# Performance work log

Hardware: AMD Instinct MI355X
Metric: run time of the kernel (lower is better)

The kernel has to match this reference:

```python
import jax, jax.numpy as jnp
import numpy as np

D_MODEL = 512
N_HEADS = 8
D_KV = 64
EPS = 1e-6
ROPE_THETA = 10000.0


def _rms_norm(x, w):
    # T5-style RMSNorm: no mean subtraction, no bias, variance in fp32.
    var = jnp.mean(x.astype(jnp.float32) ** 2, axis=-1, keepdims=True)
    return (x * jax.lax.rsqrt(var + EPS)).astype(x.dtype) * w


def _rope_cos_sin(pos, dk):
    # pos: [B, T] int -> cos/sin: [B, 1, T, dk]
    inv_freq = 1.0 / (ROPE_THETA ** (jnp.arange(0, dk, 2, dtype=jnp.float32) / dk))
    ang = pos.astype(jnp.float32)[:, :, None] * inv_freq[None, None, :]  # [B,T,dk/2]
    ang = jnp.concatenate([ang, ang], axis=-1)                            # [B,T,dk]
    return jnp.cos(ang)[:, None], jnp.sin(ang)[:, None]


def _rotate_half(x):
    h = x.shape[-1] // 2
    return jnp.concatenate([-x[..., h:], x[..., :h]], axis=-1)


def _mha(x, mask, wq, wk, wv, wo, pos=None):
    # x: [B, T, D]; mask: [B, H, T, T] additive
    B, T, _ = x.shape
    def proj(w):
        return (x @ w).reshape(B, T, N_HEADS, D_KV).transpose(0, 2, 1, 3)  # [B,H,T,dk]
    q, k, v = proj(wq), proj(wk), proj(wv)
    if pos is not None:
        cos, sin = _rope_cos_sin(pos, D_KV)
        cos, sin = cos.astype(x.dtype), sin.astype(x.dtype)
        q = q * cos + _rotate_half(q) * sin
        k = k * cos + _rotate_half(k) * sin
    scale = 1.0 / np.sqrt(D_KV)
    scores = jnp.einsum('bhqd,bhkd->bhqk', q, k) * scale + mask
    attn = jax.nn.softmax(scores.astype(jnp.float32), axis=-1).astype(scores.dtype)
    out = jnp.einsum('bhqk,bhkd->bhqd', attn, v)
    out = out.transpose(0, 2, 1, 3).reshape(B, T, N_HEADS * D_KV)
    return out @ wo


def setup_inputs() -> dict:
    key = jax.random.key(0)
    ks = jax.random.split(key, 12)
    B, T = 8, 1024
    s = 1.0 / np.sqrt(D_MODEL)
    inp = {
        'h': jax.random.normal(ks[0], (B, T, D_MODEL), dtype=jnp.float32),
        'pos': jnp.broadcast_to(jnp.arange(T, dtype=jnp.int64 if jax.config.jax_enable_x64 else jnp.int32)[None, :], (B, T)),
        't_mask': jnp.zeros((B, N_HEADS, T, T), dtype=jnp.float32),
        'g_mask': jnp.zeros((T, N_HEADS, B, B), dtype=jnp.float32),
        'ln_t_w': jnp.ones((D_MODEL,), dtype=jnp.float32),
        'ln_g_w': jnp.ones((D_MODEL,), dtype=jnp.float32),
    }
    names = ['wq_t', 'wk_t', 'wv_t', 'wo_t', 'wq_g', 'wk_g', 'wv_g', 'wo_g']
    for i, n in enumerate(names):
        inp[n] = jax.random.normal(ks[i + 1], (D_MODEL, D_MODEL), dtype=jnp.float32) * s
    return inp


def reference(h, pos, t_mask, g_mask, ln_t_w, ln_g_w,
              wq_t, wk_t, wv_t, wo_t, wq_g, wk_g, wv_g, wo_g):
    # --- time attention (over T axis, with RoPE) ---
    normed = _rms_norm(h, ln_t_w)
    attn_t = _mha(normed, t_mask, wq_t, wk_t, wv_t, wo_t, pos=pos)
    h = h + attn_t  # dropout p=0 (eval)
    # --- group attention (over B axis, no RoPE) ---
    h = h.transpose(1, 0, 2)  # [T, B, D]
    normed = _rms_norm(h, ln_g_w)
    attn_g = _mha(normed, g_mask, wq_g, wk_g, wv_g, wo_g, pos=None)
    h = h + attn_g
    return h.transpose(1, 0, 2)  # back to [B, T, D]
```

## Files before the change

kernel.cpp:

```cpp
#include <hip/hip_runtime.h>
#include <hip/hip_bf16.h>
#include <math.h>


typedef __bf16 bf16x8 __attribute__((ext_vector_type(8)));
typedef __bf16 bf16x4 __attribute__((ext_vector_type(4)));
typedef float  f32x4  __attribute__((ext_vector_type(4)));

#define LN1E4_OVER_32 0.2878231366242558f

__device__ __forceinline__ void gld16(const void* g, void* l) {
    __builtin_amdgcn_global_load_lds((const __attribute__((address_space(1))) void*)g,
                                     (__attribute__((address_space(3))) void*)l,
                                     16, 0, 0);
}

__device__ __forceinline__ int swz64(int r, int c) {
    return r * 64 + (((c + r) & 7) << 3);
}

__global__ __launch_bounds__(256) void prep_k(
    const float* __restrict__ x, const float* __restrict__ wln, __bf16* __restrict__ y,
    const float* w0, const float* w1, const float* w2, const float* w3,
    const float* w4, const float* w5, const float* w6, const float* w7,
    const float* __restrict__ gln, float* __restrict__ rmsbuf,
    __bf16* qkvT_t, __bf16* oT_t, __bf16* qkvT_g, __bf16* oT_g)
{
    __shared__ float tile[32][33];
    int bid = blockIdx.x;
    if (bid < 2048) {
        if (bid < 32) rmsbuf[bid * 256 + threadIdx.x] = 0.0f;
        int row = bid * 4 + (threadIdx.x >> 6);
        int l = threadIdx.x & 63;
        const float* xr = x + (size_t)row * 512 + l * 8;
        float4 a = *(const float4*)xr;
        float4 b = *(const float4*)(xr + 4);
        float ss = a.x*a.x + a.y*a.y + a.z*a.z + a.w*a.w
                 + b.x*b.x + b.y*b.y + b.z*b.z + b.w*b.w;
        for (int m = 1; m < 64; m <<= 1) ss += __shfl_xor(ss, m);
        float rms = rsqrtf(ss * (1.0f / 512.0f) + 1e-6f);
        float4 wa = *(const float4*)(wln + l * 8);
        float4 wb = *(const float4*)(wln + l * 8 + 4);
        bf16x8 o;
        o[0] = (__bf16)(a.x * rms * wa.x); o[1] = (__bf16)(a.y * rms * wa.y);
        o[2] = (__bf16)(a.z * rms * wa.z); o[3] = (__bf16)(a.w * rms * wa.w);
        o[4] = (__bf16)(b.x * rms * wb.x); o[5] = (__bf16)(b.y * rms * wb.y);
        o[6] = (__bf16)(b.z * rms * wb.z); o[7] = (__bf16)(b.w * rms * wb.w);
        *(bf16x8*)(y + (size_t)row * 512 + l * 8) = o;
        return;
    }
    int bid2 = bid - 2048;
    int mat = bid2 >> 8, rem = bid2 & 255;
    const float* src; __bf16* dst; int rowOff;
    switch (mat) {
        case 0: src=w0; dst=qkvT_t; rowOff=0;    break;
        case 1: src=w1; dst=qkvT_t; rowOff=512;  break;
        case 2: src=w2; dst=qkvT_t; rowOff=1024; break;
        case 3: src=w3; dst=oT_t;   rowOff=0;    break;
        case 4: src=w4; dst=qkvT_g; rowOff=0;    break;
        case 5: src=w5; dst=qkvT_g; rowOff=512;  break;
        case 6: src=w6; dst=qkvT_g; rowOff=1024; break;
        default: src=w7; dst=oT_g;  rowOff=0;    break;
    }
    bool foldG = (mat >= 4 && mat <= 6);
    int n0 = (rem & 15) * 32, k0 = (rem >> 4) * 32;
    int tt = threadIdx.x;
    int kr = tt >> 3, nc = (tt & 7) * 4;
    float4 v = *(const float4*)(src + (size_t)(k0 + kr) * 512 + n0 + nc);
    tile[kr][nc+0] = v.x; tile[kr][nc+1] = v.y; tile[kr][nc+2] = v.z; tile[kr][nc+3] = v.w;
    __syncthreads();
    int nr = tt >> 3, kc = (tt & 7) * 4;
    float g0 = 1.f, g1 = 1.f, g2 = 1.f, g3 = 1.f;
    if (foldG) {
        float4 gv = *(const float4*)(gln + k0 + kc);
        g0 = gv.x; g1 = gv.y; g2 = gv.z; g3 = gv.w;
    }
    bf16x4 o;
    o[0] = (__bf16)(tile[kc+0][nr] * g0); o[1] = (__bf16)(tile[kc+1][nr] * g1);
    o[2] = (__bf16)(tile[kc+2][nr] * g2); o[3] = (__bf16)(tile[kc+3][nr] * g3);
    *(bf16x4*)(dst + (size_t)(rowOff + n0 + nr) * 512 + k0 + kc) = o;
}

__global__ __launch_bounds__(256) void gemm_ep(
    const __bf16* __restrict__ A, const __bf16* __restrict__ Bt,
    const int* __restrict__ pos, const float* __restrict__ rmsv,
    __bf16* __restrict__ o0, __bf16* __restrict__ o1, __bf16* __restrict__ o2,
    int mode)
{
    __shared__ __bf16 smem[16384];
    __bf16* As = smem;
    __bf16* Bs = smem + 8192;
    int tid = threadIdx.x;
    int l = tid & 63, w = tid >> 6;
    int l16 = l & 15, quad = l >> 4;
    int wm = w >> 1, wn = w & 1;
    int mblk = blockIdx.x * 128, nblk = blockIdx.y * 128;
    f32x4 acc[4][4] = {};

    for (int k0 = 0; k0 < 512; k0 += 64) {
        __syncthreads();
        #pragma unroll
        for (int i = 0; i < 4; ++i) {
            int idx = i * 256 + tid;
            int row = idx >> 3, cp = idx & 7;
            int cl = (cp - row) & 7;
            gld16(A  + (size_t)(mblk + row) * 512 + k0 + cl * 8, (char*)As + (size_t)idx * 16);
            gld16(Bt + (size_t)(nblk + row) * 512 + k0 + cl * 8, (char*)Bs + (size_t)idx * 16);
        }
        __syncthreads();
        #pragma unroll
        for (int h = 0; h < 2; h++) {
            bf16x8 aF[4], bF[4];
            #pragma unroll
            for (int mt = 0; mt < 4; mt++) aF[mt] = *(bf16x8*)(As + swz64(wm * 64 + mt * 16 + l16, h * 4 + quad));
            #pragma unroll
            for (int nt = 0; nt < 4; nt++) bF[nt] = *(bf16x8*)(Bs + swz64(wn * 64 + nt * 16 + l16, h * 4 + quad));
            #pragma unroll
            for (int mt = 0; mt < 4; mt++)
                #pragma unroll
                for (int nt = 0; nt < 4; nt++)
                    acc[mt][nt] = __builtin_amdgcn_mfma_f32_16x16x32_bf16(aF[mt], bF[nt], acc[mt][nt], 0, 0, 0);
        }
    }
    __syncthreads();

    int colbase = nblk + wn * 64;
    __bf16* bw = smem + w * 1536;
    int rbrow = l >> 3, rbch = (l & 7) * 8;

    int mat = colbase >> 9;
    int hh  = (colbase & 511) >> 6;
    __bf16* dst = (mat == 0) ? o0 : (mat == 1) ? o1 : o2;
    bool isQ = (mat == 0), isV = (mat == 2);
    if (mode == 0 && !isV) {
        float f0 = __expf((float)l16        * -LN1E4_OVER_32);
        float f1 = __expf((float)(16 + l16) * -LN1E4_OVER_32);
        #pragma unroll
        for (int mt = 0; mt < 4; mt++) {
            int grow0 = mblk + wm * 64 + mt * 16;
            int b = grow0 >> 10, t0 = grow0 & 1023;
            int4 p4 = *(const int4*)&pos[grow0 + quad * 4];
            const int pa[4] = {p4.x, p4.y, p4.z, p4.w};
            #pragma unroll
            for (int r = 0; r < 4; r++) {
                float p = (float)pa[r];
                #pragma unroll
                for (int nt = 0; nt < 2; nt++) {
                    int i = nt * 16 + l16;
                    float ang = p * (nt ? f1 : f0);
                    float c, s; __sincosf(ang, &s, &c);
                    float x1 = acc[mt][nt][r], x2 = acc[mt][nt + 2][r];
                    float y1 = x1 * c - x2 * s;
                    float y2 = x2 * c + x1 * s;
                    if (isQ) { y1 *= 0.125f; y2 *= 0.125f; }
                    bw[(quad * 4 + r) * 72 + i]      = (__bf16)y1;
                    bw[(quad * 4 + r) * 72 + i + 32] = (__bf16)y2;
                }
            }
            #pragma unroll
            for (int i = 0; i < 2; ++i) {
                int rr = rbrow + i * 8;
                bf16x8 vv = *(bf16x8*)&bw[rr * 72 + rbch];
                *(bf16x8*)&dst[((size_t)(b * 8 + hh) * 1024 + t0 + rr) * 64 + rbch] = vv;
            }
        }
    } else if (mode == 0) {
        #pragma unroll
        for (int mt = 0; mt < 4; mt++) {
            #pragma unroll
            for (int nt = 0; nt < 4; nt++)
                #pragma unroll
                for (int r = 0; r < 4; r++)
                    bw[(nt * 16 + l16) * 24 + quad * 4 + r] = (__bf16)acc[mt][nt][r];
            int grow0 = mblk + wm * 64 + mt * 16;
            int b = grow0 >> 10, t0 = grow0 & 1023;
            #pragma unroll
            for (int i = 0; i < 2; ++i) {
                int li = i * 64 + l;
                int d = li >> 1, t8 = (li & 1) * 8;
                bf16x8 vv = *(bf16x8*)&bw[d * 24 + t8];
                *(bf16x8*)&dst[((size_t)(b * 8 + hh) * 64 + d) * 1024 + t0 + t8] = vv;
            }
        }
    } else {
        #pragma unroll
        for (int mt = 0; mt < 4; mt++) {
            int grow0 = mblk + wm * 64 + mt * 16;
            f32x4 ss4 = *(const f32x4*)&rmsv[grow0 + quad * 4];
            float rsq[4];
            #pragma unroll
            for (int r = 0; r < 4; r++)
                rsq[r] = rsqrtf(ss4[r] * (1.0f / 512.0f) + 1e-6f) * (isQ ? 0.125f : 1.0f);
            #pragma unroll
            for (int nt = 0; nt < 4; nt++)
                #pragma unroll
                for (int r = 0; r < 4; r++)
                    bw[(quad * 4 + r) * 72 + nt * 16 + l16] = (__bf16)(acc[mt][nt][r] * rsq[r]);
            #pragma unroll
            for (int i = 0; i < 2; ++i) {
                int rr = rbrow + i * 8;
                int grow = grow0 + rr;
                int t = grow >> 3, bq = grow & 7;
                bf16x8 vv = *(bf16x8*)&bw[rr * 72 + rbch];
                *(bf16x8*)&dst[(((size_t)t * 8 + hh) * 8 + bq) * 64 + rbch] = vv;
            }
        }
    }
}

__global__ __launch_bounds__(256) void gemm_o(
    const __bf16* __restrict__ A, const __bf16* __restrict__ Bt,
    const float* __restrict__ resid, float* __restrict__ outF,
    __bf16* __restrict__ h2b, float* __restrict__ rmsbuf, int remap)
{
    __shared__ __align__(16) char smemraw[24576];
    __bf16* As = (__bf16*)smemraw;
    __bf16* Bs = (__bf16*)(smemraw + 8192);
    int tid = threadIdx.x;
    int l = tid & 63, w = tid >> 6;
    int l16 = l & 15, quad = l >> 4;
    int mblk = blockIdx.x * 64, nblk = blockIdx.y * 128;
    f32x4 acc[8] = {};

    for (int k0 = 0; k0 < 512; k0 += 64) {
        __syncthreads();
        #pragma unroll
        for (int i = 0; i < 2; ++i) {
            int idx = i * 256 + tid;
            int row = idx >> 3, cp = idx & 7;
            int cl = (cp - row) & 7;
            gld16(A + (size_t)(mblk + row) * 512 + k0 + cl * 8, (char*)As + (size_t)idx * 16);
        }
        #pragma unroll
        for (int i = 0; i < 4; ++i) {
            int idx = i * 256 + tid;
            int row = idx >> 3, cp = idx & 7;
            int cl = (cp - row) & 7;
            gld16(Bt + (size_t)(nblk + row) * 512 + k0 + cl * 8, (char*)Bs + (size_t)idx * 16);
        }
        __syncthreads();
        #pragma unroll
        for (int h = 0; h < 2; h++) {
            bf16x8 aF = *(bf16x8*)(As + swz64(w * 16 + l16, h * 4 + quad));
            #pragma unroll
            for (int nt = 0; nt < 8; nt++) {
                bf16x8 bF = *(bf16x8*)(Bs + swz64(nt * 16 + l16, h * 4 + quad));
                acc[nt] = __builtin_amdgcn_mfma_f32_16x16x32_bf16(aF, bF, acc[nt], 0, 0, 0);
            }
        }
    }
    __syncthreads();

    float* fw = (float*)(smemraw + w * 4352);
    int grow0 = mblk + w * 16;
    float ssq[4] = {0.f, 0.f, 0.f, 0.f};
    #pragma unroll
    for (int nh = 0; nh < 2; nh++) {
        #pragma unroll
        for (int nt = 0; nt < 4; nt++)
            #pragma unroll
            for (int r = 0; r < 4; r++)
                fw[(quad * 4 + r) * 68 + nt * 16 + l16] = acc[nh * 4 + nt][r];
        #pragma unroll
        for (int i = 0; i < 4; ++i) {
            int rr = i * 4 + (l >> 4);
            int c4 = (l & 15) * 4;
            f32x4 a4 = *(f32x4*)&fw[rr * 68 + c4];
            int grow = grow0 + rr;
            int orow = remap ? (((grow & 7) << 10) + (grow >> 3)) : grow;
            size_t oi = (size_t)orow * 512 + nblk + nh * 64 + c4;
            f32x4 r4 = *(const f32x4*)&resid[oi];
            r4 += a4;
            *(f32x4*)&outF[oi] = r4;
            if (!remap) {
                int b = grow >> 10, t = grow & 1023;
                int orow2 = t * 8 + b;
                bf16x4 h4;
                h4[0] = (__bf16)r4[0]; h4[1] = (__bf16)r4[1];
                h4[2] = (__bf16)r4[2]; h4[3] = (__bf16)r4[3];
                *(bf16x4*)&h2b[(size_t)orow2 * 512 + nblk + nh * 64 + c4] = h4;
                ssq[i] += r4[0]*r4[0] + r4[1]*r4[1] + r4[2]*r4[2] + r4[3]*r4[3];
            }
        }
    }
    if (!remap) {
        #pragma unroll
        for (int i = 0; i < 4; ++i) {
            float s = ssq[i];
            s += __shfl_xor(s, 1);
            s += __shfl_xor(s, 2);
            s += __shfl_xor(s, 4);
            s += __shfl_xor(s, 8);
            if ((l & 15) == 0) {
                int grow = grow0 + i * 4 + (l >> 4);
                int orow2 = (grow & 1023) * 8 + (grow >> 10);
                atomicAdd(&rmsbuf[orow2], s);
            }
        }
    }
}

__global__ __launch_bounds__(512) void flash_t(
    const __bf16* __restrict__ q, const __bf16* __restrict__ k,
    const __bf16* __restrict__ vt, const float* __restrict__ tmask,
    __bf16* __restrict__ ctx)
{
    int bh = blockIdx.x;
    int w = threadIdx.x >> 6, l = threadIdx.x & 63;
    int l16 = l & 15, quad = l >> 4;
    int q0 = blockIdx.y * 128 + w * 16;

    __shared__ __bf16 Ks[64 * 72];
    __shared__ __bf16 Vs[64 * 72];
    __shared__ __bf16 Ps[8][16 * 72];

    bf16x8 aQ0, aQ1;
    {
        const __bf16* qp = q + ((size_t)bh * 1024 + q0 + l16) * 64 + quad * 8;
        aQ0 = *(const bf16x8*)qp;
        aQ1 = *(const bf16x8*)(qp + 32);
    }
    f32x4 o[4] = {};
    float l_acc[4] = {0.0f, 0.0f, 0.0f, 0.0f};

    const float* mrow = tmask + (size_t)bh * 1024 * 1024 + (size_t)(q0 + quad * 4) * 1024 + l16;
    float mc[16];
    #pragma unroll
    for (int r = 0; r < 4; r++)
        #pragma unroll
        for (int nt = 0; nt < 4; nt++)
            mc[r * 4 + nt] = __builtin_nontemporal_load(mrow + (size_t)r * 1024 + nt * 16);

    for (int jb = 0; jb < 1024; jb += 64) {
        __syncthreads();
        {
            int c = threadIdx.x;
            int row = c >> 3, col = (c & 7) << 3;
            *(bf16x8*)&Ks[row * 72 + col] = *(const bf16x8*)&k [((size_t)bh * 1024 + jb + row) * 64 + col];
            *(bf16x8*)&Vs[row * 72 + col] = *(const bf16x8*)&vt[((size_t)bh * 64 + row) * 1024 + jb + col];
        }
        __syncthreads();

        float mn_[16];
        {
            int jb2 = (jb + 64) & 1023;
            const float* mr2 = mrow + jb2;
            #pragma unroll
            for (int r = 0; r < 4; r++)
                #pragma unroll
                for (int nt = 0; nt < 4; nt++)
                    mn_[r * 4 + nt] = __builtin_nontemporal_load(mr2 + (size_t)r * 1024 + nt * 16);
        }

        f32x4 s[4] = {};
        #pragma unroll
        for (int nt = 0; nt < 4; nt++) {
            bf16x8 b0 = *(bf16x8*)&Ks[(nt * 16 + l16) * 72 + quad * 8];
            bf16x8 b1 = *(bf16x8*)&Ks[(nt * 16 + l16) * 72 + 32 + quad * 8];
            s[nt] = __builtin_amdgcn_mfma_f32_16x16x32_bf16(aQ0, b0, s[nt], 0, 0, 0);
            s[nt] = __builtin_amdgcn_mfma_f32_16x16x32_bf16(aQ1, b1, s[nt], 0, 0, 0);
        }
        #pragma unroll
        for (int r = 0; r < 4; r++)
            #pragma unroll
            for (int nt = 0; nt < 4; nt++) {
                float p = __expf(s[nt][r] + mc[r * 4 + nt]);
                s[nt][r] = p;
                l_acc[r] += p;
            }

        __bf16* ps = Ps[w];
        #pragma unroll
        for (int nt = 0; nt < 4; nt++)
            #pragma unroll
            for (int r = 0; r < 4; r++)
                ps[(quad * 4 + r) * 72 + nt * 16 + l16] = (__bf16)s[nt][r];
        bf16x8 aP0 = *(bf16x8*)&ps[l16 * 72 + quad * 8];
        bf16x8 aP1 = *(bf16x8*)&ps[l16 * 72 + 32 + quad * 8];
        #pragma unroll
        for (int dt = 0; dt < 4; dt++) {
            bf16x8 bv0 = *(bf16x8*)&Vs[(dt * 16 + l16) * 72 + quad * 8];
            bf16x8 bv1 = *(bf16x8*)&Vs[(dt * 16 + l16) * 72 + 32 + quad * 8];
            o[dt] = __builtin_amdgcn_mfma_f32_16x16x32_bf16(aP0, bv0, o[dt], 0, 0, 0);
            o[dt] = __builtin_amdgcn_mfma_f32_16x16x32_bf16(aP1, bv1, o[dt], 0, 0, 0);
        }

        #pragma unroll
        for (int i = 0; i < 16; i++) mc[i] = mn_[i];
    }

    float l_i[4];
    #pragma unroll
    for (int r = 0; r < 4; r++) {
        float rs = l_acc[r];
        rs += __shfl_xor(rs, 1);
        rs += __shfl_xor(rs, 2);
        rs += __shfl_xor(rs, 4);
        rs += __shfl_xor(rs, 8);
        l_i[r] = rs;
    }

    int b = bh >> 3, h = bh & 7;
    __bf16* ps = Ps[w];
    #pragma unroll
    for (int dt = 0; dt < 4; dt++)
        #pragma unroll
        for (int r = 0; r < 4; r++)
            ps[(quad * 4 + r) * 72 + dt * 16 + l16] = (__bf16)(o[dt][r] / l_i[r]);
    int rbrow = l >> 3, rbch = (l & 7) * 8;
    #pragma unroll
    for (int i = 0; i < 2; ++i) {
        int rr = rbrow + i * 8;
        bf16x8 vv = *(bf16x8*)&ps[rr * 72 + rbch];
        *(bf16x8*)&ctx[((size_t)b * 1024 + q0 + rr) * 512 + h * 64 + rbch] = vv;
    }
}

__global__ __launch_bounds__(256) void group_attn(
    const __bf16* __restrict__ qg, const __bf16* __restrict__ kg,
    const __bf16* __restrict__ vg, const float* __restrict__ gmask,
    __bf16* __restrict__ ctxg)
{
    int tid = blockIdx.x * 256 + threadIdx.x;
    int t = tid >> 6, h = (tid >> 3) & 7, bq = tid & 7;
    size_t base = ((size_t)t * 8 + h) * 512;

    float qv[64];
    #pragma unroll
    for (int d0 = 0; d0 < 64; d0 += 8) {
        bf16x8 qq = *(const bf16x8*)&qg[base + (size_t)bq * 64 + d0];
        #pragma unroll
        for (int u = 0; u < 8; u++) qv[d0 + u] = (float)qq[u];
    }
    float s[8];
    #pragma unroll
    for (int j = 0; j < 8; j++) {
        float acc = 0.0f;
        #pragma unroll
        for (int d0 = 0; d0 < 64; d0 += 8) {
            bf16x8 kk = *(const bf16x8*)&kg[base + (size_t)j * 64 + d0];
            #pragma unroll
            for (int u = 0; u < 8; u++) acc += qv[d0 + u] * (float)kk[u];
        }
        s[j] = acc + gmask[(((size_t)t * 8 + h) * 8 + bq) * 8 + j];
    }
    float mx = s[0];
    #pragma unroll
    for (int j = 1; j < 8; j++) mx = fmaxf(mx, s[j]);
    float sum = 0.0f;
    #pragma unroll
    for (int j = 0; j < 8; j++) { s[j] = __expf(s[j] - mx); sum += s[j]; }
    float inv = 1.0f / sum;

    #pragma unroll
    for (int d0 = 0; d0 < 64; d0 += 8) {
        float o8[8] = {};
        #pragma unroll
        for (int j = 0; j < 8; j++) {
            bf16x8 vv = *(const bf16x8*)&vg[base + (size_t)j * 64 + d0];
            float pj = s[j];
            #pragma unroll
            for (int u = 0; u < 8; u++) o8[u] += pj * (float)vv[u];
        }
        bf16x8 ob;
        #pragma unroll
        for (int u = 0; u < 8; u++) ob[u] = (__bf16)(o8[u] * inv);
        *(bf16x8*)&ctxg[((size_t)t * 8 + bq) * 512 + h * 64 + d0] = ob;
    }
}

extern "C" void kernel_launch(void* const* d_in, const int* in_sizes, int n_in,
                              void* d_out, int out_size, void* d_ws, size_t ws_size,
                              hipStream_t stream)
{
    const float* h      = (const float*)d_in[0];
    const int*   pos    = (const int*)  d_in[1];
    const float* t_mask = (const float*)d_in[2];
    const float* g_mask = (const float*)d_in[3];
    const float* ln_t_w = (const float*)d_in[4];
    const float* ln_g_w = (const float*)d_in[5];
    const float* wq_t = (const float*)d_in[6];
    const float* wk_t = (const float*)d_in[7];
    const float* wv_t = (const float*)d_in[8];
    const float* wo_t = (const float*)d_in[9];
    const float* wq_g = (const float*)d_in[10];
    const float* wk_g = (const float*)d_in[11];
    const float* wv_g = (const float*)d_in[12];
    const float* wo_g = (const float*)d_in[13];
    float* out = (float*)d_out;

    char* ws = (char*)d_ws;
    const size_t MB = 1ull << 20;
    __bf16* qkvT_t = (__bf16*)ws;
    __bf16* oT_t   = qkvT_t + 786432;
    __bf16* qkvT_g = qkvT_t + 1048576;
    __bf16* oT_g   = qkvT_t + 1835008;
    __bf16* normed = (__bf16*)(ws + 4 * MB);
    __bf16* qb     = (__bf16*)(ws + 12 * MB);
    __bf16* kb     = (__bf16*)(ws + 20 * MB);
    __bf16* vb     = (__bf16*)(ws + 28 * MB);
    __bf16* ctx    = (__bf16*)(ws + 36 * MB);
    float*  h2     = (float*) (ws + 44 * MB);
    float*  rmsbuf = (float*) (ws + 60 * MB);
    __bf16* h2b    = (__bf16*)(ws + 61 * MB);

    prep_k<<<4096, 256, 0, stream>>>(h, ln_t_w, normed,
        wq_t, wk_t, wv_t, wo_t, wq_g, wk_g, wv_g, wo_g,
        ln_g_w, rmsbuf, qkvT_t, oT_t, qkvT_g, oT_g);
    gemm_ep<<<dim3(64, 12), 256, 0, stream>>>(normed, qkvT_t, pos, nullptr, qb, kb, vb, 0);
    flash_t<<<dim3(64, 8), 512, 0, stream>>>(qb, kb, vb, t_mask, ctx);
    gemm_o<<<dim3(128, 4), 256, 0, stream>>>(ctx, oT_t, h, h2, h2b, rmsbuf, 0);

    gemm_ep<<<dim3(64, 12), 256, 0, stream>>>(h2b, qkvT_g, nullptr, rmsbuf, qb, kb, vb, 2);
    group_attn<<<256, 256, 0, stream>>>(qb, kb, vb, g_mask, ctx);
    gemm_o<<<dim3(128, 4), 256, 0, stream>>>(ctx, oT_g, h2, out, nullptr, nullptr, 1);
}
```

Before: 499.0 us.

## Precompute RoPE table, prefetch K/V in flash loop, vectorize V-transpose stores

Adds extra blocks to the prep kernel that compute a cos/sin table per position, and the QKV GEMM epilogue reads it instead of evaluating sincos per element. The flash attention loop now register-prefetches the next K/V tile while the current one is processed, so global load latency overlaps compute. The V-transpose epilogue writes packed bf16x4 to shared memory, and the final normalization uses a reciprocal multiply instead of a divide. The trade-offs are extra table memory traffic in the GEMM epilogue and higher register pressure in the flash kernel.

Result: no change. 496.7 us (-0.5%).

```diff
diff --git a/kernel.cpp b/kernel.cpp
--- a/kernel.cpp
+++ b/kernel.cpp
@@ -24,7 +24,8 @@
     const float* w0, const float* w1, const float* w2, const float* w3,
     const float* w4, const float* w5, const float* w6, const float* w7,
     const float* __restrict__ gln, float* __restrict__ rmsbuf,
-    __bf16* qkvT_t, __bf16* oT_t, __bf16* qkvT_g, __bf16* oT_g)
+    __bf16* qkvT_t, __bf16* oT_t, __bf16* qkvT_g, __bf16* oT_g,
+    const int* __restrict__ pos, float2* __restrict__ rope)
 {
     __shared__ float tile[32][33];
     int bid = blockIdx.x;
@@ -49,6 +50,17 @@
         *(bf16x8*)(y + (size_t)row * 512 + l * 8) = o;
         return;
     }
+    if (bid >= 4096) {
+        int idx = bid - 4096;
+        int r = threadIdx.x >> 5, i = threadIdx.x & 31;
+        int row = idx * 8 + r;
+        float p = (float)pos[row];
+        float f = __expf((float)i * -LN1E4_OVER_32);
+        float s, c;
+        __sincosf(p * f, &s, &c);
+        rope[(size_t)row * 32 + i] = make_float2(c, s);
+        return;
+    }
     int bid2 = bid - 2048;
     int mat = bid2 >> 8, rem = bid2 & 255;
     const float* src; __bf16* dst; int rowOff;
@@ -83,7 +95,7 @@
 
 __global__ __launch_bounds__(256) void gemm_ep(
     const __bf16* __restrict__ A, const __bf16* __restrict__ Bt,
-    const int* __restrict__ pos, const float* __restrict__ rmsv,
+    const float2* __restrict__ rope, const float* __restrict__ rmsv,
     __bf16* __restrict__ o0, __bf16* __restrict__ o1, __bf16* __restrict__ o2,
     int mode)
 {
@@ -133,25 +145,20 @@
     __bf16* dst = (mat == 0) ? o0 : (mat == 1) ? o1 : o2;
     bool isQ = (mat == 0), isV = (mat == 2);
     if (mode == 0 && !isV) {
-        float f0 = __expf((float)l16        * -LN1E4_OVER_32);
-        float f1 = __expf((float)(16 + l16) * -LN1E4_OVER_32);
         #pragma unroll
         for (int mt = 0; mt < 4; mt++) {
             int grow0 = mblk + wm * 64 + mt * 16;
             int b = grow0 >> 10, t0 = grow0 & 1023;
-            int4 p4 = *(const int4*)&pos[grow0 + quad * 4];
-            const int pa[4] = {p4.x, p4.y, p4.z, p4.w};
             #pragma unroll
             for (int r = 0; r < 4; r++) {
-                float p = (float)pa[r];
+                const float2* tp = rope + (size_t)(grow0 + quad * 4 + r) * 32;
                 #pragma unroll
                 for (int nt = 0; nt < 2; nt++) {
                     int i = nt * 16 + l16;
-                    float ang = p * (nt ? f1 : f0);
-                    float c, s; __sincosf(ang, &s, &c);
+                    float2 cs = tp[i];
                     float x1 = acc[mt][nt][r], x2 = acc[mt][nt + 2][r];
-                    float y1 = x1 * c - x2 * s;
-                    float y2 = x2 * c + x1 * s;
+                    float y1 = x1 * cs.x - x2 * cs.y;
+                    float y2 = x2 * cs.x + x1 * cs.y;
                     if (isQ) { y1 *= 0.125f; y2 *= 0.125f; }
                     bw[(quad * 4 + r) * 72 + i]      = (__bf16)y1;
                     bw[(quad * 4 + r) * 72 + i + 32] = (__bf16)y2;
@@ -168,10 +175,12 @@
         #pragma unroll
         for (int mt = 0; mt < 4; mt++) {
             #pragma unroll
-            for (int nt = 0; nt < 4; nt++)
+            for (int nt = 0; nt < 4; nt++) {
+                bf16x4 o4;
                 #pragma unroll
-                for (int r = 0; r < 4; r++)
-                    bw[(nt * 16 + l16) * 24 + quad * 4 + r] = (__bf16)acc[mt][nt][r];
+                for (int r = 0; r < 4; r++) o4[r] = (__bf16)acc[mt][nt][r];
+                *(bf16x4*)&bw[(nt * 16 + l16) * 24 + quad * 4] = o4;
+            }
             int grow0 = mblk + wm * 64 + mt * 16;
             int b = grow0 >> 10, t0 = grow0 & 1023;
             #pragma unroll
@@ -331,15 +340,22 @@
         for (int nt = 0; nt < 4; nt++)
             mc[r * 4 + nt] = __builtin_nontemporal_load(mrow + (size_t)r * 1024 + nt * 16);
 
+    int c = threadIdx.x;
+    int srow = c >> 3, scol = (c & 7) << 3;
+    const __bf16* kbase = k  + ((size_t)bh * 1024 + srow) * 64 + scol;
+    const __bf16* vbase = vt + ((size_t)bh * 64 + srow) * 1024 + scol;
+    bf16x8 kreg = *(const bf16x8*)kbase;
+    bf16x8 vreg = *(const bf16x8*)vbase;
+
     for (int jb = 0; jb < 1024; jb += 64) {
         __syncthreads();
-        {
-            int c = threadIdx.x;
-            int row = c >> 3, col = (c & 7) << 3;
-            *(bf16x8*)&Ks[row * 72 + col] = *(const bf16x8*)&k [((size_t)bh * 1024 + jb + row) * 64 + col];
-            *(bf16x8*)&Vs[row * 72 + col] = *(const bf16x8*)&vt[((size_t)bh * 64 + row) * 1024 + jb + col];
-        }
+        *(bf16x8*)&Ks[srow * 72 + scol] = kreg;
+        *(bf16x8*)&Vs[srow * 72 + scol] = vreg;
         __syncthreads();
+        if (jb + 64 < 1024) {
+            kreg = *(const bf16x8*)(kbase + (size_t)(jb + 64) * 64);
+            vreg = *(const bf16x8*)(vbase + (jb + 64));
+        }
 
         float mn_[16];
         {
@@ -389,7 +405,7 @@
         for (int i = 0; i < 16; i++) mc[i] = mn_[i];
     }
 
-    float l_i[4];
+    float inv_l[4];
     #pragma unroll
     for (int r = 0; r < 4; r++) {
         float rs = l_acc[r];
@@ -397,7 +413,7 @@
         rs += __shfl_xor(rs, 2);
         rs += __shfl_xor(rs, 4);
         rs += __shfl_xor(rs, 8);
-        l_i[r] = rs;
+        inv_l[r] = 1.0f / rs;
     }
 
     int b = bh >> 3, h = bh & 7;
@@ -406,7 +422,7 @@
     for (int dt = 0; dt < 4; dt++)
         #pragma unroll
         for (int r = 0; r < 4; r++)
-            ps[(quad * 4 + r) * 72 + dt * 16 + l16] = (__bf16)(o[dt][r] / l_i[r]);
+            ps[(quad * 4 + r) * 72 + dt * 16 + l16] = (__bf16)(o[dt][r] * inv_l[r]);
     int rbrow = l >> 3, rbch = (l & 7) * 8;
     #pragma unroll
     for (int i = 0; i < 2; ++i) {
@@ -503,11 +519,12 @@
     float*  h2     = (float*) (ws + 44 * MB);
     float*  rmsbuf = (float*) (ws + 60 * MB);
     __bf16* h2b    = (__bf16*)(ws + 61 * MB);
-
-    prep_k<<<4096, 256, 0, stream>>>(h, ln_t_w, normed,
+    float2* rope   = (float2*)(ws + 70 * MB);
+
+    prep_k<<<5120, 256, 0, stream>>>(h, ln_t_w, normed,
         wq_t, wk_t, wv_t, wo_t, wq_g, wk_g, wv_g, wo_g,
-        ln_g_w, rmsbuf, qkvT_t, oT_t, qkvT_g, oT_g);
-    gemm_ep<<<dim3(64, 12), 256, 0, stream>>>(normed, qkvT_t, pos, nullptr, qb, kb, vb, 0);
+        ln_g_w, rmsbuf, qkvT_t, oT_t, qkvT_g, oT_g, pos, rope);
+    gemm_ep<<<dim3(64, 12), 256, 0, stream>>>(normed, qkvT_t, rope, nullptr, qb, kb, vb, 0);
     flash_t<<<dim3(64, 8), 512, 0, stream>>>(qb, kb, vb, t_mask, ctx);
     gemm_o<<<dim3(128, 4), 256, 0, stream>>>(ctx, oT_t, h, h2, h2b, rmsbuf, 0);
 
```
